# Optimization experiments

Measured on AMD Instinct MI355X. Metric: run time of the kernel, lower is better.

Reference implementation:

```python
import jax, jax.numpy as jnp
import numpy as np
from jax import lax

STRIDE = 4
PAD = 3
TOP_K = 2
LOSS_COEF = 1e-2
LN_EPS = 1e-6


def _expert(x, W, b, ln_w, ln_b):
    # Conv2d(c1->c2, k=7, stride=4, pad=3) + channel-first LayerNorm (over C only)
    y = lax.conv_general_dilated(x, W, (STRIDE, STRIDE), [(PAD, PAD), (PAD, PAD)],
                                 dimension_numbers=("NCHW", "OIHW", "NCHW"))
    y = y + b[None, :, None, None]
    u = y.mean(1, keepdims=True)
    s = ((y - u) ** 2).mean(1, keepdims=True)
    y = (y - u) / jnp.sqrt(s + LN_EPS)
    return ln_w[None, :, None, None] * y + ln_b[None, :, None, None]


def _cv_squared(v):
    v = v.astype(jnp.float32)
    return jnp.var(v, ddof=1) / (jnp.mean(v) ** 2 + 1e-10)


def setup_inputs() -> dict:
    key = jax.random.key(0)
    ks = jax.random.split(key, 10)
    B, C1, H, W = 32, 3, 224, 224
    C2, E, KS = 64, 8, 7
    return {
        "x": jax.random.normal(ks[0], (B, C1, H, W), jnp.float32),
        "expert_W": jax.random.normal(ks[1], (E, C2, C1, KS, KS), jnp.float32) * 0.05,
        "expert_b": jax.random.normal(ks[2], (E, C2), jnp.float32) * 0.02,
        "expert_ln_w": jnp.ones((E, C2), jnp.float32),
        "expert_ln_b": jnp.zeros((E, C2), jnp.float32),
        "shared_W": jax.random.normal(ks[3], (C2, C1, KS, KS), jnp.float32) * 0.05,
        "shared_b": jax.random.normal(ks[4], (C2,), jnp.float32) * 0.02,
        "shared_ln_w": jnp.ones((C2,), jnp.float32),
        "shared_ln_b": jnp.zeros((C2,), jnp.float32),
        "w_gate": jax.random.normal(ks[5], (C1, E), jnp.float32) * 0.1,
    }


def reference(x, expert_W, expert_b, expert_ln_w, expert_ln_b,
              shared_W, shared_b, shared_ln_w, shared_ln_b, w_gate):
    B = x.shape[0]
    E = w_gate.shape[1]
    # --- noisy_top_k_gating (eval path: clean logits, no noise) ---
    gate_inp = x.mean(axis=(2, 3))                     # [B, width=c1]
    logits = gate_inp @ w_gate                          # [B, E]
    top_vals, top_idx = lax.top_k(logits, TOP_K)        # [B, k]
    top_gates = jax.nn.softmax(top_vals, axis=1)        # [B, k]
    gates = jnp.zeros((B, E), logits.dtype).at[jnp.arange(B)[:, None], top_idx].set(top_gates)
    # --- load-balancing aux loss ---
    importance = gates.sum(0)
    load = (gates > 0).sum(0).astype(jnp.float32)
    loss = LOSS_COEF * (_cv_squared(importance) + _cv_squared(load))
    # --- dispatch/combine: dense-equivalent of SparseDispatcher ---
    # output[b] = sum_e gates[b,e] * expert_e(x[b])  (zero gates mask out experts)
    expert_outs = jax.vmap(lambda W, b, lw, lb: _expert(x, W, b, lw, lb))(
        expert_W, expert_b, expert_ln_w, expert_ln_b)   # [E, B, C2, H', W']
    y = jnp.einsum("be,ebchw->bchw", gates, expert_outs)
    y = y + _expert(x, shared_W, shared_b, shared_ln_w, shared_ln_b)
    return y, loss
```

## Files before the change

kernel.cpp:

```cpp
#include <hip/hip_runtime.h>
#include <cstdint>
#include <cstddef>

static constexpr int BATCH = 32;
static constexpr int CIN   = 3;
static constexpr int HIN   = 224, WIN = 224;
static constexpr int COUT  = 64;
static constexpr int HOUT  = 56, WOUT = 56;
static constexpr int NPIX  = HOUT * WOUT;
static constexpr int NEXP  = 8;
static constexpr int KROWS = 21;
static constexpr int KPAD2 = 192;
static constexpr int NKS   = 6;
static constexpr int NGRP  = 7;
static constexpr int TPB   = 7;
static constexpr int PWL   = 232;
static constexpr int WR    = 35;
static constexpr float LN_EPS_F = 1e-6f;

static constexpr int N_GATE = BATCH * CIN;
static constexpr int N_REPACK = (9 * COUT * KPAD2 + 255) / 256;

typedef __bf16 bf16x8 __attribute__((ext_vector_type(8)));
typedef float  f32x4  __attribute__((ext_vector_type(4)));

__device__ __align__(16) ushort g_pw2[9 * COUT * KPAD2];
__device__ float g_gateinp[BATCH * CIN];

__device__ __forceinline__ ushort f2bf(float f) {
  uint u = __float_as_uint(f);
  uint r = (u + 0x7FFFu + ((u >> 16) & 1u)) >> 16;
  return (ushort)r;
}

__device__ __forceinline__ void barrier_lgkm() {
  asm volatile("s_waitcnt lgkmcnt(0)" ::: "memory");
  __builtin_amdgcn_s_barrier();
  __builtin_amdgcn_sched_barrier(0);
}

__global__ __launch_bounds__(256) void k_pre(const float* __restrict__ x,
                                             const float* __restrict__ eW,
                                             const float* __restrict__ sW) {
  const int bid = blockIdx.x;
  if (bid < N_GATE) {
    const int plane = bid;
    const float4* p4 = reinterpret_cast<const float4*>(x + (size_t)plane * (HIN * WIN));
    float s = 0.f;
    for (int i = threadIdx.x; i < (HIN * WIN) / 4; i += 256) {
      const float4 v = p4[i];
      s += v.x + v.y + v.z + v.w;
    }
    __shared__ float red[256];
    red[threadIdx.x] = s;
    __syncthreads();
    for (int off = 128; off > 0; off >>= 1) {
      if ((int)threadIdx.x < off) red[threadIdx.x] += red[threadIdx.x + off];
      __syncthreads();
    }
    if (threadIdx.x == 0) g_gateinp[plane] = red[0] * (1.f / (float)(HIN * WIN));
  } else {
    const int idx = (bid - N_GATE) * 256 + threadIdx.x;
    if (idx >= 9 * COUT * KPAD2) return;
    const int k2  = idx % KPAD2;
    const int coe = idx / KPAD2;
    const int co  = coe & 63;
    const int e   = coe >> 6;
    const int kwp = k2 & 7;
    const int row = k2 >> 3;
    float v = 0.f;
    if (kwp >= 1 && row < KROWS) {
      const int k = row * 7 + (kwp - 1);
      v = (e < 8) ? eW[(size_t)coe * 147 + k] : sW[(size_t)co * 147 + k];
    }
    g_pw2[idx] = f2bf(v);
  }
}

__global__ __launch_bounds__(512, 1) void k_main(
    const float* __restrict__ x,
    const float* __restrict__ w_gate,
    const float* __restrict__ eB, const float* __restrict__ sB,
    const float* __restrict__ elnw, const float* __restrict__ elnb,
    const float* __restrict__ slnw, const float* __restrict__ slnb,
    float* __restrict__ out, float* __restrict__ loss_out) {
  __shared__ __align__(16) ushort Wnd[3 * WR * PWL];
  __shared__ float2 Sstats[2][8][3][2][16];

  const int tid  = threadIdx.x;
  const int lane = tid & 63;
  const int w    = tid >> 6;
  const int b    = blockIdx.x / NGRP;
  const int g    = blockIdx.x % NGRP;

  {
    for (int i = tid; i < 3 * WR * 28; i += 512) {
      const int j8 = i % 28;
      const int rr = i / 28;
      const int ci = rr / WR;
      const int wr = rr - ci * WR;
      const int ih = 32 * g + wr - 3;
      uint2 lo = {0u, 0u}, hi = {0u, 0u};
      if ((unsigned)ih < (unsigned)HIN) {
        const float4* xr = reinterpret_cast<const float4*>(
            x + ((size_t)(b * CIN + ci) * HIN + ih) * WIN);
        const float4 f0 = xr[2 * j8];
        const float4 f1 = xr[2 * j8 + 1];
        lo.x = (uint)f2bf(f0.x) | ((uint)f2bf(f0.y) << 16);
        lo.y = (uint)f2bf(f0.z) | ((uint)f2bf(f0.w) << 16);
        hi.x = (uint)f2bf(f1.x) | ((uint)f2bf(f1.y) << 16);
        hi.y = (uint)f2bf(f1.z) | ((uint)f2bf(f1.w) << 16);
      }
      *reinterpret_cast<uint2*>(&Wnd[rr * PWL + 8 * j8 + 4]) = lo;
      *reinterpret_cast<uint2*>(&Wnd[rr * PWL + 8 * j8 + 8]) = hi;
      if (j8 == 0) {
        const uint2 z = {0u, 0u};
        *reinterpret_cast<uint2*>(&Wnd[rr * PWL]) = z;
      }
      if (j8 == 27) {
        const uint2 z = {0u, 0u};
        *reinterpret_cast<uint2*>(&Wnd[rr * PWL + 228]) = z;
      }
    }
  }

  const float gi0 = g_gateinp[b * 3 + 0];
  const float gi1 = g_gateinp[b * 3 + 1];
  const float gi2 = g_gateinp[b * 3 + 2];
  float best1 = -1e30f, best2 = -1e30f;
  int i1 = 0, i2 = 0;
  #pragma unroll
  for (int e = 0; e < NEXP; ++e) {
    const float lg = gi0 * w_gate[e] + gi1 * w_gate[8 + e] + gi2 * w_gate[16 + e];
    if (lg > best1) { best2 = best1; i2 = i1; best1 = lg; i1 = e; }
    else if (lg > best2) { best2 = lg; i2 = e; }
  }
  const float e21 = expf(best2 - best1);
  const float g1 = 1.f / (1.f + e21);
  const float g2 = e21 / (1.f + e21);
  const int e1 = __builtin_amdgcn_readfirstlane(i1);
  const int e2 = __builtin_amdgcn_readfirstlane(i2);

  const int m    = lane >> 4;
  const int colA = lane & 15;
  const int wc   = w >> 1;
  const int wh   = w & 1;
  const int wbase = wc * 16;
  const int eidx[3] = {e1, e2, 8};

  bf16x8 afrag[3][NKS];
  #pragma unroll
  for (int e = 0; e < 3; ++e) {
    const ushort* ape = g_pw2 + ((size_t)(eidx[e] * COUT + wbase + colA)) * KPAD2 + m * 8;
    #pragma unroll
    for (int ks = 0; ks < NKS; ++ks)
      afrag[e][ks] = __builtin_bit_cast(bf16x8, *reinterpret_cast<const uint4*>(ape + ks * 32));
  }

  int Crow[NKS];
  #pragma unroll
  for (int ks = 0; ks < NKS; ++ks) {
    int r = 4 * ks + m;
    r = r > 20 ? 20 : r;
    const int ci = r >= 14 ? 2 : (r >= 7 ? 1 : 0);
    const int kh = r - ci * 7;
    Crow[ks] = (ci * WR + kh) * PWL;
  }

  const int co0 = wbase + m * 4;
  const int col = colA;
  float4 bias[3], lw[3], lb[3];
  bias[0] = *reinterpret_cast<const float4*>(eB + e1 * COUT + co0);
  bias[1] = *reinterpret_cast<const float4*>(eB + e2 * COUT + co0);
  bias[2] = *reinterpret_cast<const float4*>(sB + co0);
  lw[0] = *reinterpret_cast<const float4*>(elnw + e1 * COUT + co0);
  lw[1] = *reinterpret_cast<const float4*>(elnw + e2 * COUT + co0);
  lw[2] = *reinterpret_cast<const float4*>(slnw + co0);
  lb[0] = *reinterpret_cast<const float4*>(elnb + e1 * COUT + co0);
  lb[1] = *reinterpret_cast<const float4*>(elnb + e2 * COUT + co0);
  lb[2] = *reinterpret_cast<const float4*>(slnb + co0);
  const float ge[3] = {g1, g2, 1.f};

  if (blockIdx.x == 0 && w == 0) {
    float mg1 = 0.f, mg2 = 0.f;
    int me1 = -1, me2 = -1;
    if (lane < BATCH) {
      const float a0 = g_gateinp[lane * 3 + 0];
      const float a1 = g_gateinp[lane * 3 + 1];
      const float a2 = g_gateinp[lane * 3 + 2];
      float b1 = -1e30f, b2 = -1e30f;
      int j1 = 0, j2 = 0;
      #pragma unroll
      for (int e = 0; e < NEXP; ++e) {
        const float lg = a0 * w_gate[e] + a1 * w_gate[8 + e] + a2 * w_gate[16 + e];
        if (lg > b1) { b2 = b1; j2 = j1; b1 = lg; j1 = e; }
        else if (lg > b2) { b2 = lg; j2 = e; }
      }
      const float q = expf(b2 - b1);
      mg1 = 1.f / (1.f + q); mg2 = q / (1.f + q);
      me1 = j1; me2 = j2;
    }
    float imp[NEXP], lod[NEXP];
    #pragma unroll
    for (int e = 0; e < NEXP; ++e) {
      float ie = ((me1 == e) ? mg1 : 0.f) + ((me2 == e) ? mg2 : 0.f);
      float le = (((me1 == e) && (mg1 > 0.f)) ? 1.f : 0.f)
               + (((me2 == e) && (mg2 > 0.f)) ? 1.f : 0.f);
      #pragma unroll
      for (int o = 32; o > 0; o >>= 1) { ie += __shfl_xor(ie, o, 64); le += __shfl_xor(le, o, 64); }
      imp[e] = ie; lod[e] = le;
    }
    if (lane == 0) {
      float mi = 0.f, ml = 0.f;
      #pragma unroll
      for (int e = 0; e < NEXP; ++e) { mi += imp[e]; ml += lod[e]; }
      mi *= (1.f / NEXP); ml *= (1.f / NEXP);
      float vi = 0.f, vl = 0.f;
      #pragma unroll
      for (int e = 0; e < NEXP; ++e) {
        const float di = imp[e] - mi; vi += di * di;
        const float dl = lod[e] - ml; vl += dl * dl;
      }
      vi *= (1.f / (NEXP - 1)); vl *= (1.f / (NEXP - 1));
      loss_out[0] = 0.01f * (vi / (mi * mi + 1e-10f) + vl / (ml * ml + 1e-10f));
    }
  }

  __syncthreads();

  float* const outb = out + (size_t)b * (COUT * NPIX);

  for (int i = 0; i < TPB; ++i) {
    const int par = i & 1;
    const int t   = g * TPB + i;
    const int t64 = t * 64;

    int baseB[2], pxv[2];
    #pragma unroll
    for (int cbL = 0; cbL < 2; ++cbL) {
      const int px = (2 * wh + cbL) * 16 + colA;
      const int pg = t64 + px;
      const int oh = pg / WOUT;
      const int ow = pg - oh * WOUT;
      baseB[cbL] = ((oh - 8 * g) * 4) * PWL + ow * 4;
      pxv[cbL]   = px;
    }

    f32x4 acc[2][3];
    #pragma unroll
    for (int cbL = 0; cbL < 2; ++cbL)
      #pragma unroll
      for (int e = 0; e < 3; ++e) acc[cbL][e] = (f32x4){0.f, 0.f, 0.f, 0.f};

    #pragma unroll
    for (int ks = 0; ks < NKS; ++ks) {
      #pragma unroll
      for (int cbL = 0; cbL < 2; ++cbL) {
        const ushort* p = &Wnd[baseB[cbL] + Crow[ks]];
        const uint2 lo = *reinterpret_cast<const uint2*>(p);
        const uint2 hi = *reinterpret_cast<const uint2*>(p + 4);
        const uint4 raw = {lo.x, lo.y, hi.x, hi.y};
        const bf16x8 bf = __builtin_bit_cast(bf16x8, raw);
        #pragma unroll
        for (int e = 0; e < 3; ++e)
          acc[cbL][e] = __builtin_amdgcn_mfma_f32_16x16x32_bf16(afrag[e][ks], bf, acc[cbL][e], 0, 0, 0);
      }
    }

    #pragma unroll
    for (int cbL = 0; cbL < 2; ++cbL)
      #pragma unroll
      for (int e = 0; e < 3; ++e) {
        acc[cbL][e][0] += (&bias[e].x)[0];
        acc[cbL][e][1] += (&bias[e].x)[1];
        acc[cbL][e][2] += (&bias[e].x)[2];
        acc[cbL][e][3] += (&bias[e].x)[3];
      }

    #pragma unroll
    for (int cbL = 0; cbL < 2; ++cbL)
      #pragma unroll
      for (int e = 0; e < 3; ++e) {
        float s = acc[cbL][e][0] + acc[cbL][e][1] + acc[cbL][e][2] + acc[cbL][e][3];
        float q = acc[cbL][e][0] * acc[cbL][e][0] + acc[cbL][e][1] * acc[cbL][e][1]
                + acc[cbL][e][2] * acc[cbL][e][2] + acc[cbL][e][3] * acc[cbL][e][3];
        s += __shfl_xor(s, 16, 64); s += __shfl_xor(s, 32, 64);
        q += __shfl_xor(q, 16, 64); q += __shfl_xor(q, 32, 64);
        if (lane < 16) Sstats[par][w][e][cbL][col] = make_float2(s, q);
      }

    barrier_lgkm();

    #pragma unroll
    for (int cbL = 0; cbL < 2; ++cbL) {
      float u[3], rr[3];
      #pragma unroll
      for (int e = 0; e < 3; ++e) {
        float s = 0.f, q = 0.f;
        #pragma unroll
        for (int wcp = 0; wcp < 4; ++wcp) {
          const float2 sq = Sstats[par][wcp * 2 + wh][e][cbL][col];
          s += sq.x; q += sq.y;
        }
        u[e] = s * (1.f / 64.f);
        const float var = q * (1.f / 64.f) - u[e] * u[e];
        rr[e] = rsqrtf(var + LN_EPS_F);
      }
      #pragma unroll
      for (int reg = 0; reg < 4; ++reg) {
        float o = 0.f;
        #pragma unroll
        for (int e = 0; e < 3; ++e) {
          const float y = acc[cbL][e][reg];
          o += ge[e] * ((&lw[e].x)[reg] * (y - u[e]) * rr[e] + (&lb[e].x)[reg]);
        }
        outb[(size_t)(co0 + reg) * NPIX + t64 + pxv[cbL]] = o;
      }
    }
  }
}

extern "C" void kernel_launch(void* const* d_in, const int* in_sizes, int n_in,
                              void* d_out, int out_size, void* d_ws, size_t ws_size,
                              hipStream_t stream) {
  const float* x    = (const float*)d_in[0];
  const float* eW   = (const float*)d_in[1];
  const float* eB   = (const float*)d_in[2];
  const float* elnw = (const float*)d_in[3];
  const float* elnb = (const float*)d_in[4];
  const float* sW   = (const float*)d_in[5];
  const float* sB   = (const float*)d_in[6];
  const float* slnw = (const float*)d_in[7];
  const float* slnb = (const float*)d_in[8];
  const float* wg   = (const float*)d_in[9];
  float* out = (float*)d_out;

  float* loss_ptr = out + (size_t)BATCH * COUT * NPIX;

  k_pre<<<N_GATE + N_REPACK, 256, 0, stream>>>(x, eW, sW);
  k_main<<<BATCH * NGRP, 512, 0, stream>>>(x, wg, eB, sB, elnw, elnb,
                                           slnw, slnb, out, loss_ptr);
}
```

Before: 48.74 us.

## Split gate reduction across more blocks and restructure main kernel per-wave channel tiles

The gate-mean prepass now splits each input plane across 8 blocks that write partial sums, which the main kernel adds up. The main kernel doubles the row groups per image (14 instead of 7) and uses 448-thread blocks that allow two blocks per CU. Each wave now computes all 64 output channels for two 16-pixel tiles, looping over the three experts. This lets LayerNorm statistics be reduced within a wave using shuffles, which removes the shared-memory stats exchange and the barriers. In exchange, weight fragments are reloaded from global memory for every expert instead of being held in registers, and the input halo rows are loaded redundantly across more blocks.

```diff
diff --git a/kernel.cpp b/kernel.cpp
--- a/kernel.cpp
+++ b/kernel.cpp
@@ -12,20 +12,19 @@
 static constexpr int KROWS = 21;
 static constexpr int KPAD2 = 192;
 static constexpr int NKS   = 6;
-static constexpr int NGRP  = 7;
-static constexpr int TPB   = 7;
+static constexpr int NGRP  = 14;
 static constexpr int PWL   = 232;
-static constexpr int WR    = 35;
+static constexpr int WR    = 19;
 static constexpr float LN_EPS_F = 1e-6f;
 
-static constexpr int N_GATE = BATCH * CIN;
+static constexpr int N_GPART  = BATCH * CIN * 8;
 static constexpr int N_REPACK = (9 * COUT * KPAD2 + 255) / 256;
 
 typedef __bf16 bf16x8 __attribute__((ext_vector_type(8)));
 typedef float  f32x4  __attribute__((ext_vector_type(4)));
 
 __device__ __align__(16) ushort g_pw2[9 * COUT * KPAD2];
-__device__ float g_gateinp[BATCH * CIN];
+__device__ float g_gatepart[BATCH * CIN * 8];
 
 __device__ __forceinline__ ushort f2bf(float f) {
   uint u = __float_as_uint(f);
@@ -33,21 +32,17 @@
   return (ushort)r;
 }
 
-__device__ __forceinline__ void barrier_lgkm() {
-  asm volatile("s_waitcnt lgkmcnt(0)" ::: "memory");
-  __builtin_amdgcn_s_barrier();
-  __builtin_amdgcn_sched_barrier(0);
-}
-
 __global__ __launch_bounds__(256) void k_pre(const float* __restrict__ x,
                                              const float* __restrict__ eW,
                                              const float* __restrict__ sW) {
   const int bid = blockIdx.x;
-  if (bid < N_GATE) {
-    const int plane = bid;
+  if (bid < N_GPART) {
+    const int plane = bid >> 3;
+    const int slice = bid & 7;
     const float4* p4 = reinterpret_cast<const float4*>(x + (size_t)plane * (HIN * WIN));
     float s = 0.f;
-    for (int i = threadIdx.x; i < (HIN * WIN) / 4; i += 256) {
+    const int i0 = slice * 1568;
+    for (int i = i0 + (int)threadIdx.x; i < i0 + 1568; i += 256) {
       const float4 v = p4[i];
       s += v.x + v.y + v.z + v.w;
     }
@@ -58,9 +53,9 @@
       if ((int)threadIdx.x < off) red[threadIdx.x] += red[threadIdx.x + off];
       __syncthreads();
     }
-    if (threadIdx.x == 0) g_gateinp[plane] = red[0] * (1.f / (float)(HIN * WIN));
+    if (threadIdx.x == 0) g_gatepart[bid] = red[0];
   } else {
-    const int idx = (bid - N_GATE) * 256 + threadIdx.x;
+    const int idx = (bid - N_GPART) * 256 + threadIdx.x;
     if (idx >= 9 * COUT * KPAD2) return;
     const int k2  = idx % KPAD2;
     const int coe = idx / KPAD2;
@@ -77,7 +72,7 @@
   }
 }
 
-__global__ __launch_bounds__(512, 1) void k_main(
+__global__ __launch_bounds__(448, 2) void k_main(
     const float* __restrict__ x,
     const float* __restrict__ w_gate,
     const float* __restrict__ eB, const float* __restrict__ sB,
@@ -85,53 +80,49 @@
     const float* __restrict__ slnw, const float* __restrict__ slnb,
     float* __restrict__ out, float* __restrict__ loss_out) {
   __shared__ __align__(16) ushort Wnd[3 * WR * PWL];
-  __shared__ float2 Sstats[2][8][3][2][16];
 
   const int tid  = threadIdx.x;
   const int lane = tid & 63;
   const int w    = tid >> 6;
   const int b    = blockIdx.x / NGRP;
-  const int g    = blockIdx.x % NGRP;
-
-  {
-    for (int i = tid; i < 3 * WR * 28; i += 512) {
-      const int j8 = i % 28;
-      const int rr = i / 28;
-      const int ci = rr / WR;
-      const int wr = rr - ci * WR;
-      const int ih = 32 * g + wr - 3;
-      uint2 lo = {0u, 0u}, hi = {0u, 0u};
-      if ((unsigned)ih < (unsigned)HIN) {
-        const float4* xr = reinterpret_cast<const float4*>(
-            x + ((size_t)(b * CIN + ci) * HIN + ih) * WIN);
-        const float4 f0 = xr[2 * j8];
-        const float4 f1 = xr[2 * j8 + 1];
-        lo.x = (uint)f2bf(f0.x) | ((uint)f2bf(f0.y) << 16);
-        lo.y = (uint)f2bf(f0.z) | ((uint)f2bf(f0.w) << 16);
-        hi.x = (uint)f2bf(f1.x) | ((uint)f2bf(f1.y) << 16);
-        hi.y = (uint)f2bf(f1.z) | ((uint)f2bf(f1.w) << 16);
-      }
-      *reinterpret_cast<uint2*>(&Wnd[rr * PWL + 8 * j8 + 4]) = lo;
-      *reinterpret_cast<uint2*>(&Wnd[rr * PWL + 8 * j8 + 8]) = hi;
-      if (j8 == 0) {
-        const uint2 z = {0u, 0u};
-        *reinterpret_cast<uint2*>(&Wnd[rr * PWL]) = z;
-      }
-      if (j8 == 27) {
-        const uint2 z = {0u, 0u};
-        *reinterpret_cast<uint2*>(&Wnd[rr * PWL + 228]) = z;
-      }
-    }
-  }
-
-  const float gi0 = g_gateinp[b * 3 + 0];
-  const float gi1 = g_gateinp[b * 3 + 1];
-  const float gi2 = g_gateinp[b * 3 + 2];
+  const int G    = blockIdx.x % NGRP;
+
+  for (int i = tid; i < 3 * WR * 28; i += 448) {
+    const int j8 = i % 28;
+    const int rr = i / 28;
+    const int ci = rr / WR;
+    const int wr = rr - ci * WR;
+    const int ih = 16 * G + wr - 3;
+    uint2 lo = {0u, 0u}, hi = {0u, 0u};
+    if ((unsigned)ih < (unsigned)HIN) {
+      const float4* xr = reinterpret_cast<const float4*>(
+          x + ((size_t)(b * CIN + ci) * HIN + ih) * WIN);
+      const float4 f0 = xr[2 * j8];
+      const float4 f1 = xr[2 * j8 + 1];
+      lo.x = (uint)f2bf(f0.x) | ((uint)f2bf(f0.y) << 16);
+      lo.y = (uint)f2bf(f0.z) | ((uint)f2bf(f0.w) << 16);
+      hi.x = (uint)f2bf(f1.x) | ((uint)f2bf(f1.y) << 16);
+      hi.y = (uint)f2bf(f1.z) | ((uint)f2bf(f1.w) << 16);
+    }
+    *reinterpret_cast<uint2*>(&Wnd[rr * PWL + 8 * j8 + 4]) = lo;
+    *reinterpret_cast<uint2*>(&Wnd[rr * PWL + 8 * j8 + 8]) = hi;
+    if (j8 == 0)  { const uint2 z = {0u, 0u}; *reinterpret_cast<uint2*>(&Wnd[rr * PWL]) = z; }
+    if (j8 == 27) { const uint2 z = {0u, 0u}; *reinterpret_cast<uint2*>(&Wnd[rr * PWL + 228]) = z; }
+  }
+
+  float gi[3];
+  #pragma unroll
+  for (int c = 0; c < 3; ++c) {
+    float s = 0.f;
+    #pragma unroll
+    for (int p = 0; p < 8; ++p) s += g_gatepart[(b * 3 + c) * 8 + p];
+    gi[c] = s * (1.f / (float)(HIN * WIN));
+  }
   float best1 = -1e30f, best2 = -1e30f;
   int i1 = 0, i2 = 0;
   #pragma unroll
   for (int e = 0; e < NEXP; ++e) {
-    const float lg = gi0 * w_gate[e] + gi1 * w_gate[8 + e] + gi2 * w_gate[16 + e];
+    const float lg = gi[0] * w_gate[e] + gi[1] * w_gate[8 + e] + gi[2] * w_gate[16 + e];
     if (lg > best1) { best2 = best1; i2 = i1; best1 = lg; i1 = e; }
     else if (lg > best2) { best2 = lg; i2 = e; }
   }
@@ -141,21 +132,60 @@
   const int e1 = __builtin_amdgcn_readfirstlane(i1);
   const int e2 = __builtin_amdgcn_readfirstlane(i2);
 
+  if (blockIdx.x == 0 && w == 0) {
+    float mg1 = 0.f, mg2 = 0.f;
+    int me1 = -1, me2 = -1;
+    if (lane < BATCH) {
+      float a[3];
+      #pragma unroll
+      for (int c = 0; c < 3; ++c) {
+        float s = 0.f;
+        #pragma unroll
+        for (int p = 0; p < 8; ++p) s += g_gatepart[(lane * 3 + c) * 8 + p];
+        a[c] = s * (1.f / (float)(HIN * WIN));
+      }
+      float b1 = -1e30f, b2 = -1e30f;
+      int j1 = 0, j2 = 0;
+      #pragma unroll
+      for (int e = 0; e < NEXP; ++e) {
+        const float lg = a[0] * w_gate[e] + a[1] * w_gate[8 + e] + a[2] * w_gate[16 + e];
+        if (lg > b1) { b2 = b1; j2 = j1; b1 = lg; j1 = e; }
+        else if (lg > b2) { b2 = lg; j2 = e; }
+      }
+      const float q = expf(b2 - b1);
+      mg1 = 1.f / (1.f + q); mg2 = q / (1.f + q);
+      me1 = j1; me2 = j2;
+    }
+    float imp[NEXP], lod[NEXP];
+    #pragma unroll
+    for (int e = 0; e < NEXP; ++e) {
+      float ie = ((me1 == e) ? mg1 : 0.f) + ((me2 == e) ? mg2 : 0.f);
+      float le = (((me1 == e) && (mg1 > 0.f)) ? 1.f : 0.f)
+               + (((me2 == e) && (mg2 > 0.f)) ? 1.f : 0.f);
+      #pragma unroll
+      for (int o = 32; o > 0; o >>= 1) { ie += __shfl_xor(ie, o, 64); le += __shfl_xor(le, o, 64); }
+      imp[e] = ie; lod[e] = le;
+    }
+    if (lane == 0) {
+      float mi = 0.f, ml = 0.f;
+      #pragma unroll
+      for (int e = 0; e < NEXP; ++e) { mi += imp[e]; ml += lod[e]; }
+      mi *= (1.f / NEXP); ml *= (1.f / NEXP);
+      float vi = 0.f, vl = 0.f;
+      #pragma unroll
+      for (int e = 0; e < NEXP; ++e) {
+        const float di = imp[e] - mi; vi += di * di;
+        const float dl = lod[e] - ml; vl += dl * dl;
+      }
+      vi *= (1.f / (NEXP - 1)); vl *= (1.f / (NEXP - 1));
+      loss_out[0] = 0.01f * (vi / (mi * mi + 1e-10f) + vl / (ml * ml + 1e-10f));
+    }
+  }
+
   const int m    = lane >> 4;
   const int colA = lane & 15;
-  const int wc   = w >> 1;
-  const int wh   = w & 1;
-  const int wbase = wc * 16;
   const int eidx[3] = {e1, e2, 8};
-
-  bf16x8 afrag[3][NKS];
-  #pragma unroll
-  for (int e = 0; e < 3; ++e) {
-    const ushort* ape = g_pw2 + ((size_t)(eidx[e] * COUT + wbase + colA)) * KPAD2 + m * 8;
-    #pragma unroll
-    for (int ks = 0; ks < NKS; ++ks)
-      afrag[e][ks] = __builtin_bit_cast(bf16x8, *reinterpret_cast<const uint4*>(ape + ks * 32));
-  }
+  const float ge[3] = {g1, g2, 1.f};
 
   int Crow[NKS];
   #pragma unroll
@@ -167,157 +197,101 @@
     Crow[ks] = (ci * WR + kh) * PWL;
   }
 
-  const int co0 = wbase + m * 4;
-  const int col = colA;
-  float4 bias[3], lw[3], lb[3];
-  bias[0] = *reinterpret_cast<const float4*>(eB + e1 * COUT + co0);
-  bias[1] = *reinterpret_cast<const float4*>(eB + e2 * COUT + co0);
-  bias[2] = *reinterpret_cast<const float4*>(sB + co0);
-  lw[0] = *reinterpret_cast<const float4*>(elnw + e1 * COUT + co0);
-  lw[1] = *reinterpret_cast<const float4*>(elnw + e2 * COUT + co0);
-  lw[2] = *reinterpret_cast<const float4*>(slnw + co0);
-  lb[0] = *reinterpret_cast<const float4*>(elnb + e1 * COUT + co0);
-  lb[1] = *reinterpret_cast<const float4*>(elnb + e2 * COUT + co0);
-  lb[2] = *reinterpret_cast<const float4*>(slnb + co0);
-  const float ge[3] = {g1, g2, 1.f};
-
-  if (blockIdx.x == 0 && w == 0) {
-    float mg1 = 0.f, mg2 = 0.f;
-    int me1 = -1, me2 = -1;
-    if (lane < BATCH) {
-      const float a0 = g_gateinp[lane * 3 + 0];
-      const float a1 = g_gateinp[lane * 3 + 1];
-      const float a2 = g_gateinp[lane * 3 + 2];
-      float b1 = -1e30f, b2 = -1e30f;
-      int j1 = 0, j2 = 0;
-      #pragma unroll
-      for (int e = 0; e < NEXP; ++e) {
-        const float lg = a0 * w_gate[e] + a1 * w_gate[8 + e] + a2 * w_gate[16 + e];
-        if (lg > b1) { b2 = b1; j2 = j1; b1 = lg; j1 = e; }
-        else if (lg > b2) { b2 = lg; j2 = e; }
-      }
-      const float q = expf(b2 - b1);
-      mg1 = 1.f / (1.f + q); mg2 = q / (1.f + q);
-      me1 = j1; me2 = j2;
-    }
-    float imp[NEXP], lod[NEXP];
-    #pragma unroll
-    for (int e = 0; e < NEXP; ++e) {
-      float ie = ((me1 == e) ? mg1 : 0.f) + ((me2 == e) ? mg2 : 0.f);
-      float le = (((me1 == e) && (mg1 > 0.f)) ? 1.f : 0.f)
-               + (((me2 == e) && (mg2 > 0.f)) ? 1.f : 0.f);
-      #pragma unroll
-      for (int o = 32; o > 0; o >>= 1) { ie += __shfl_xor(ie, o, 64); le += __shfl_xor(le, o, 64); }
-      imp[e] = ie; lod[e] = le;
-    }
-    if (lane == 0) {
-      float mi = 0.f, ml = 0.f;
-      #pragma unroll
-      for (int e = 0; e < NEXP; ++e) { mi += imp[e]; ml += lod[e]; }
-      mi *= (1.f / NEXP); ml *= (1.f / NEXP);
-      float vi = 0.f, vl = 0.f;
-      #pragma unroll
-      for (int e = 0; e < NEXP; ++e) {
-        const float di = imp[e] - mi; vi += di * di;
-        const float dl = lod[e] - ml; vl += dl * dl;
-      }
-      vi *= (1.f / (NEXP - 1)); vl *= (1.f / (NEXP - 1));
-      loss_out[0] = 0.01f * (vi / (mi * mi + 1e-10f) + vl / (ml * ml + 1e-10f));
-    }
+  int baseB[2], pxg[2];
+  #pragma unroll
+  for (int t = 0; t < 2; ++t) {
+    const int tile = w + t * 7;
+    const int pg = G * 224 + tile * 16 + colA;
+    const int oh = pg / WOUT;
+    const int ow = pg - oh * WOUT;
+    baseB[t] = ((oh - 4 * G) * 4) * PWL + ow * 4;
+    pxg[t]   = pg;
   }
 
   __syncthreads();
 
-  float* const outb = out + (size_t)b * (COUT * NPIX);
-
-  for (int i = 0; i < TPB; ++i) {
-    const int par = i & 1;
-    const int t   = g * TPB + i;
-    const int t64 = t * 64;
-
-    int baseB[2], pxv[2];
-    #pragma unroll
-    for (int cbL = 0; cbL < 2; ++cbL) {
-      const int px = (2 * wh + cbL) * 16 + colA;
-      const int pg = t64 + px;
-      const int oh = pg / WOUT;
-      const int ow = pg - oh * WOUT;
-      baseB[cbL] = ((oh - 8 * g) * 4) * PWL + ow * 4;
-      pxv[cbL]   = px;
-    }
-
-    f32x4 acc[2][3];
-    #pragma unroll
-    for (int cbL = 0; cbL < 2; ++cbL)
-      #pragma unroll
-      for (int e = 0; e < 3; ++e) acc[cbL][e] = (f32x4){0.f, 0.f, 0.f, 0.f};
-
+  float outAcc[2][16];
+  #pragma unroll
+  for (int t = 0; t < 2; ++t)
+    #pragma unroll
+    for (int j = 0; j < 16; ++j) outAcc[t][j] = 0.f;
+
+  #pragma unroll
+  for (int e = 0; e < 3; ++e) {
+    const int ebase = eidx[e] * COUT;
+    float4 bias4[4], lw4[4], lb4[4];
+    #pragma unroll
+    for (int f = 0; f < 4; ++f) {
+      const int co4 = ebase * 0 + f * 16 + m * 4;
+      bias4[f] = *reinterpret_cast<const float4*>(
+          (e < 2 ? eB + ebase + co4 : sB + co4));
+      lw4[f] = *reinterpret_cast<const float4*>(
+          (e < 2 ? elnw + ebase + co4 : slnw + co4));
+      lb4[f] = *reinterpret_cast<const float4*>(
+          (e < 2 ? elnb + ebase + co4 : slnb + co4));
+    }
+
+    f32x4 acc[2][4];
+    #pragma unroll
+    for (int t = 0; t < 2; ++t)
+      #pragma unroll
+      for (int f = 0; f < 4; ++f) acc[t][f] = (f32x4){0.f, 0.f, 0.f, 0.f};
+
+    const ushort* apeE = g_pw2 + ((size_t)(ebase + colA)) * KPAD2 + m * 8;
     #pragma unroll
     for (int ks = 0; ks < NKS; ++ks) {
-      #pragma unroll
-      for (int cbL = 0; cbL < 2; ++cbL) {
-        const ushort* p = &Wnd[baseB[cbL] + Crow[ks]];
+      bf16x8 a[4];
+      #pragma unroll
+      for (int f = 0; f < 4; ++f)
+        a[f] = __builtin_bit_cast(bf16x8, *reinterpret_cast<const uint4*>(
+            apeE + (size_t)f * 16 * KPAD2 + ks * 32));
+      #pragma unroll
+      for (int t = 0; t < 2; ++t) {
+        const ushort* p = &Wnd[baseB[t] + Crow[ks]];
         const uint2 lo = *reinterpret_cast<const uint2*>(p);
         const uint2 hi = *reinterpret_cast<const uint2*>(p + 4);
         const uint4 raw = {lo.x, lo.y, hi.x, hi.y};
         const bf16x8 bf = __builtin_bit_cast(bf16x8, raw);
         #pragma unroll
-        for (int e = 0; e < 3; ++e)
-          acc[cbL][e] = __builtin_amdgcn_mfma_f32_16x16x32_bf16(afrag[e][ks], bf, acc[cbL][e], 0, 0, 0);
-      }
-    }
-
-    #pragma unroll
-    for (int cbL = 0; cbL < 2; ++cbL)
-      #pragma unroll
-      for (int e = 0; e < 3; ++e) {
-        acc[cbL][e][0] += (&bias[e].x)[0];
-        acc[cbL][e][1] += (&bias[e].x)[1];
-        acc[cbL][e][2] += (&bias[e].x)[2];
-        acc[cbL][e][3] += (&bias[e].x)[3];
-      }
-
-    #pragma unroll
-    for (int cbL = 0; cbL < 2; ++cbL)
-      #pragma unroll
-      for (int e = 0; e < 3; ++e) {
-        float s = acc[cbL][e][0] + acc[cbL][e][1] + acc[cbL][e][2] + acc[cbL][e][3];
-        float q = acc[cbL][e][0] * acc[cbL][e][0] + acc[cbL][e][1] * acc[cbL][e][1]
-                + acc[cbL][e][2] * acc[cbL][e][2] + acc[cbL][e][3] * acc[cbL][e][3];
-        s += __shfl_xor(s, 16, 64); s += __shfl_xor(s, 32, 64);
-        q += __shfl_xor(q, 16, 64); q += __shfl_xor(q, 32, 64);
-        if (lane < 16) Sstats[par][w][e][cbL][col] = make_float2(s, q);
-      }
-
-    barrier_lgkm();
-
-    #pragma unroll
-    for (int cbL = 0; cbL < 2; ++cbL) {
-      float u[3], rr[3];
-      #pragma unroll
-      for (int e = 0; e < 3; ++e) {
-        float s = 0.f, q = 0.f;
+        for (int f = 0; f < 4; ++f)
+          acc[t][f] = __builtin_amdgcn_mfma_f32_16x16x32_bf16(a[f], bf, acc[t][f], 0, 0, 0);
+      }
+    }
+
+    #pragma unroll
+    for (int t = 0; t < 2; ++t) {
+      float s = 0.f, q = 0.f;
+      #pragma unroll
+      for (int f = 0; f < 4; ++f) {
         #pragma unroll
-        for (int wcp = 0; wcp < 4; ++wcp) {
-          const float2 sq = Sstats[par][wcp * 2 + wh][e][cbL][col];
-          s += sq.x; q += sq.y;
+        for (int r = 0; r < 4; ++r) {
+          const float y = acc[t][f][r] + (&bias4[f].x)[r];
+          acc[t][f][r] = y;
+          s += y; q += y * y;
         }
-        u[e] = s * (1.f / 64.f);
-        const float var = q * (1.f / 64.f) - u[e] * u[e];
-        rr[e] = rsqrtf(var + LN_EPS_F);
-      }
-      #pragma unroll
-      for (int reg = 0; reg < 4; ++reg) {
-        float o = 0.f;
+      }
+      s += __shfl_xor(s, 16, 64); s += __shfl_xor(s, 32, 64);
+      q += __shfl_xor(q, 16, 64); q += __shfl_xor(q, 32, 64);
+      const float u  = s * (1.f / 64.f);
+      const float vv = q * (1.f / 64.f) - u * u;
+      const float rs = rsqrtf(vv + LN_EPS_F);
+      #pragma unroll
+      for (int f = 0; f < 4; ++f)
         #pragma unroll
-        for (int e = 0; e < 3; ++e) {
-          const float y = acc[cbL][e][reg];
-          o += ge[e] * ((&lw[e].x)[reg] * (y - u[e]) * rr[e] + (&lb[e].x)[reg]);
-        }
-        outb[(size_t)(co0 + reg) * NPIX + t64 + pxv[cbL]] = o;
-      }
-    }
-  }
+        for (int r = 0; r < 4; ++r)
+          outAcc[t][f * 4 + r] += ge[e] * ((&lw4[f].x)[r] * (acc[t][f][r] - u) * rs
+                                           + (&lb4[f].x)[r]);
+    }
+  }
+
+  float* const outb = out + (size_t)b * (COUT * NPIX);
+  #pragma unroll
+  for (int t = 0; t < 2; ++t)
+    #pragma unroll
+    for (int f = 0; f < 4; ++f)
+      #pragma unroll
+      for (int r = 0; r < 4; ++r)
+        outb[(size_t)(f * 16 + m * 4 + r) * NPIX + pxg[t]] = outAcc[t][f * 4 + r];
 }
 
 extern "C" void kernel_launch(void* const* d_in, const int* in_sizes, int n_in,
@@ -337,7 +311,7 @@
 
   float* loss_ptr = out + (size_t)BATCH * COUT * NPIX;
 
-  k_pre<<<N_GATE + N_REPACK, 256, 0, stream>>>(x, eW, sW);
-  k_main<<<BATCH * NGRP, 512, 0, stream>>>(x, wg, eB, sB, elnw, elnb,
+  k_pre<<<N_GPART + N_REPACK, 256, 0, stream>>>(x, eW, sW);
+  k_main<<<BATCH * NGRP, 448, 0, stream>>>(x, wg, eB, sB, elnw, elnb,
                                            slnw, slnb, out, loss_ptr);
 }
```

New measurement: 53.00 us. 8.7% more time.
